# Performance work log

Measured on AMD Instinct MI355X. Metric: run time of the kernel, lower is better.

The kernel has to match this reference:

```python
import jax, jax.numpy as jnp
import numpy as np

DIM = 128
N = 8192
E = 262144
EPS = 1e-8  # torch.cosine_similarity eps


def setup_inputs() -> dict:
    key = jax.random.key(0)
    k1, k2, k3, k4 = jax.random.split(key, 4)
    x = jax.random.normal(k1, (N, DIM), dtype=jnp.float32)
    edge_index = jax.random.randint(k2, (2, E), 0, N, dtype=jnp.int32)
    # GCNConv parameters: linear weight (glorot-ish) and bias
    W_gcn = jax.random.normal(k3, (DIM, DIM), dtype=jnp.float32) / np.sqrt(DIM)
    b_gcn = jnp.zeros((DIM,), dtype=jnp.float32)
    return {"x": x, "edge_index": edge_index, "W_gcn": W_gcn, "b_gcn": b_gcn}


def _cosine_attention(x):
    # torch.cosine_similarity(x.unsqueeze(1), x.unsqueeze(0), dim=-1)
    # == (x @ x.T) / max(||x_i|| * ||x_j||, eps)
    nrm = jnp.sqrt(jnp.sum(x * x, axis=-1))                      # [N]
    denom = jnp.maximum(nrm[:, None] * nrm[None, :], EPS)        # [N, N]
    sim = (x @ x.T) / denom                                      # [N, N]
    return jax.nn.sigmoid(sim @ x)                               # [N, dim]


def _gcn_conv(x, edge_index, W, b):
    n = x.shape[0]
    xw = x @ W                                                   # [N, dim]
    # add self-loops
    loops = jnp.arange(n, dtype=edge_index.dtype)
    row = jnp.concatenate([edge_index[0], loops])                # source
    col = jnp.concatenate([edge_index[1], loops])                # target
    # symmetric normalization: deg computed on target nodes
    deg = jax.ops.segment_sum(jnp.ones_like(col, dtype=x.dtype), col, num_segments=n)
    dis = jnp.where(deg > 0, jax.lax.rsqrt(jnp.maximum(deg, 1.0)), 0.0)
    dis = jnp.where(deg > 0, deg ** -0.5, 0.0)
    norm = dis[row] * dis[col]                                   # [E+N]
    msgs = xw[row] * norm[:, None]                               # [E+N, dim]
    out = jax.ops.segment_sum(msgs, col, num_segments=n)         # [N, dim]
    return out + b


def reference(x, edge_index, W_gcn, b_gcn):
    att = _cosine_attention(x)
    g = _gcn_conv(x, edge_index, W_gcn, b_gcn)
    return g * att
```

## Files before the change

### kernel.cpp

```cpp
#include <hip/hip_runtime.h>
#include <math.h>

#define NN   8192
#define DIM  128
#define NE   262144
#define XB   128
#define HBH  64
#define HEB  (NE / HBH)
#define PBP  64
#define PEB  (NE / PBP)
#define RWB  32
#define BK   16
#define XSS  132
#define SMEMF 8448

static __device__ __forceinline__ unsigned short f2bf(float f) {
  unsigned int u = __float_as_uint(f);
  return (unsigned short)((u + 0x7FFFu + ((u >> 16) & 1u)) >> 16);
}
static __device__ __forceinline__ float bf2f(unsigned int h) {
  return __uint_as_float(h << 16);
}


static __device__ void ph_xtx(int u, int tid, float* smem,
    const float* __restrict__ x, float* __restrict__ rinv,
    float* __restrict__ Mpart) {
  float* xs  = smem;
  float* rvs = smem + 64 * DIM;
  int row0 = u * 64;
  const float4* xsrc = (const float4*)(x + (size_t)row0 * DIM);
  float4* xdst = (float4*)xs;
  #pragma unroll
  for (int i = 0; i < 8; ++i) xdst[tid + 256 * i] = xsrc[tid + 256 * i];
  __syncthreads();
  int rr = tid >> 2, q = tid & 3;
  const float4* xr = (const float4*)&xs[rr * DIM + q * 32];
  float ss = 0.f;
  #pragma unroll
  for (int i = 0; i < 8; ++i) {
    float4 v = xr[i];
    ss += v.x * v.x + v.y * v.y + v.z * v.z + v.w * v.w;
  }
  ss += __shfl_xor(ss, 1);
  ss += __shfl_xor(ss, 2);
  if (q == 0) { float rv = 1.0f / sqrtf(ss); rvs[rr] = rv; rinv[row0 + rr] = rv; }
  __syncthreads();

  int ty = tid >> 4, tx = tid & 15;
  float acc[8][8];
  #pragma unroll
  for (int i = 0; i < 8; ++i)
    #pragma unroll
    for (int j = 0; j < 8; ++j) acc[i][j] = 0.f;
  #pragma unroll 2
  for (int r = 0; r < 64; ++r) {
    float4 a0 = *(const float4*)&xs[r * DIM + ty * 4];
    float4 a1 = *(const float4*)&xs[r * DIM + 64 + ty * 4];
    float4 b0 = *(const float4*)&xs[r * DIM + tx * 4];
    float4 b1 = *(const float4*)&xs[r * DIM + 64 + tx * 4];
    float rv = rvs[r];
    float a[8] = {a0.x * rv, a0.y * rv, a0.z * rv, a0.w * rv,
                  a1.x * rv, a1.y * rv, a1.z * rv, a1.w * rv};
    float b[8] = {b0.x, b0.y, b0.z, b0.w, b1.x, b1.y, b1.z, b1.w};
    #pragma unroll
    for (int i = 0; i < 8; ++i)
      #pragma unroll
      for (int j = 0; j < 8; ++j) acc[i][j] += a[i] * b[j];
  }
  float* o = Mpart + (size_t)u * (DIM * DIM);
  #pragma unroll
  for (int i = 0; i < 8; ++i) {
    int row = (i < 4) ? (ty * 4 + i) : (64 + ty * 4 + (i - 4));
    *(float4*)&o[row * DIM + tx * 4]      = make_float4(acc[i][0], acc[i][1], acc[i][2], acc[i][3]);
    *(float4*)&o[row * DIM + 64 + tx * 4] = make_float4(acc[i][4], acc[i][5], acc[i][6], acc[i][7]);
  }
}

static __device__ void ph_hist(int h, int tid, int* ldeg,
    const int* __restrict__ ei, int* __restrict__ gcnt, int* __restrict__ slot) {
  int4* lz = (int4*)ldeg;
  #pragma unroll
  for (int i = tid; i < NN / 4; i += 256) lz[i] = make_int4(0, 0, 0, 0);
  __syncthreads();
  int e0 = h * HEB + tid * 16;
  int4 c0 = *(const int4*)(ei + NE + e0);
  int4 c1 = *(const int4*)(ei + NE + e0 + 4);
  int4 c2 = *(const int4*)(ei + NE + e0 + 8);
  int4 c3 = *(const int4*)(ei + NE + e0 + 12);
  int r0  = atomicAdd(&ldeg[c0.x], 1);
  int r1  = atomicAdd(&ldeg[c0.y], 1);
  int r2  = atomicAdd(&ldeg[c0.z], 1);
  int r3  = atomicAdd(&ldeg[c0.w], 1);
  int r4  = atomicAdd(&ldeg[c1.x], 1);
  int r5  = atomicAdd(&ldeg[c1.y], 1);
  int r6  = atomicAdd(&ldeg[c1.z], 1);
  int r7  = atomicAdd(&ldeg[c1.w], 1);
  int r8  = atomicAdd(&ldeg[c2.x], 1);
  int r9  = atomicAdd(&ldeg[c2.y], 1);
  int r10 = atomicAdd(&ldeg[c2.z], 1);
  int r11 = atomicAdd(&ldeg[c2.w], 1);
  int r12 = atomicAdd(&ldeg[c3.x], 1);
  int r13 = atomicAdd(&ldeg[c3.y], 1);
  int r14 = atomicAdd(&ldeg[c3.z], 1);
  int r15 = atomicAdd(&ldeg[c3.w], 1);
  __syncthreads();
  int binb = tid * 32;
  #pragma unroll
  for (int i = 0; i < 8; ++i) {
    int4 v = *(int4*)&ldeg[binb + i * 4];
    if (v.x) ldeg[binb + i * 4 + 0] = atomicAdd(&gcnt[binb + i * 4 + 0], v.x);
    if (v.y) ldeg[binb + i * 4 + 1] = atomicAdd(&gcnt[binb + i * 4 + 1], v.y);
    if (v.z) ldeg[binb + i * 4 + 2] = atomicAdd(&gcnt[binb + i * 4 + 2], v.z);
    if (v.w) ldeg[binb + i * 4 + 3] = atomicAdd(&gcnt[binb + i * 4 + 3], v.w);
  }
  __syncthreads();
  int4 s0 = make_int4(ldeg[c0.x] + r0,  ldeg[c0.y] + r1,  ldeg[c0.z] + r2,  ldeg[c0.w] + r3);
  int4 s1 = make_int4(ldeg[c1.x] + r4,  ldeg[c1.y] + r5,  ldeg[c1.z] + r6,  ldeg[c1.w] + r7);
  int4 s2 = make_int4(ldeg[c2.x] + r8,  ldeg[c2.y] + r9,  ldeg[c2.z] + r10, ldeg[c2.w] + r11);
  int4 s3 = make_int4(ldeg[c3.x] + r12, ldeg[c3.y] + r13, ldeg[c3.z] + r14, ldeg[c3.w] + r15);
  *(int4*)(slot + e0)      = s0;
  *(int4*)(slot + e0 + 4)  = s1;
  *(int4*)(slot + e0 + 8)  = s2;
  *(int4*)(slot + e0 + 12) = s3;
}

static __device__ void ph_mred(int u, int tid, float* smem,
    const float* __restrict__ Mpart, float* __restrict__ Mmat) {
  int j0 = u * 64;
  int jj = tid & 63, sub = tid >> 6;
  const float* mp = Mpart + (size_t)(sub * 32) * (DIM * DIM) + j0;
  float s = 0.f;
  #pragma unroll 4
  for (int k = 0; k < 32; ++k) s += mp[(size_t)k * (DIM * DIM) + jj];
  smem[sub * 64 + jj] = s;
  __syncthreads();
  if (tid < 64)
    Mmat[j0 + tid] = smem[tid] + smem[64 + tid] + smem[128 + tid] + smem[192 + tid];
}

static __device__ void ph_scan(int tid, int* wsum,
    const int* __restrict__ gcnt, int* __restrict__ offs, float* __restrict__ dis) {
  int lane = tid & 63, wave = tid >> 6;
  const int4* g4 = (const int4*)gcnt;
  int s = 0;
  #pragma unroll
  for (int i = 0; i < 8; ++i) { int4 v = g4[tid * 8 + i]; s += v.x + v.y + v.z + v.w; }
  int sc = s;
  #pragma unroll
  for (int off = 1; off < 64; off <<= 1) {
    int v = __shfl_up(sc, off);
    if (lane >= off) sc += v;
  }
  if (lane == 63) wsum[wave] = sc;
  __syncthreads();
  if (wave == 0 && lane < 4) {
    int v = wsum[lane];
    #pragma unroll
    for (int off = 1; off < 4; off <<= 1) {
      int u = __shfl_up(v, off);
      if (lane >= off) v += u;
    }
    wsum[lane] = v;
  }
  __syncthreads();
  int run = (wave ? wsum[wave - 1] : 0) + sc - s;
  #pragma unroll
  for (int i = 0; i < 8; ++i) {
    int4 v = g4[tid * 8 + i];
    int4 o;
    o.x = run; run += v.x;
    o.y = run; run += v.y;
    o.z = run; run += v.z;
    o.w = run; run += v.w;
    *(int4*)&offs[tid * 32 + i * 4] = o;
    float4 d;
    d.x = rsqrtf((float)(v.x + 1)); d.y = rsqrtf((float)(v.y + 1));
    d.z = rsqrtf((float)(v.z + 1)); d.w = rsqrtf((float)(v.w + 1));
    *(float4*)&dis[tid * 32 + i * 4] = d;
  }
}

static __device__ void ph_gemm(int u, int tid, float* smem,
    const float* __restrict__ x, const float* __restrict__ W,
    const float* __restrict__ Mmat, const float* __restrict__ rinv,
    const float* __restrict__ dis, unsigned short* __restrict__ xws,
    float* __restrict__ att) {
  float* xs  = smem;
  float* Wl  = smem + 4224;
  float* Ml  = smem + 6272;
  float* rvs = smem + 8320;
  float* dss = smem + 8352;
  int row0 = u * RWB;
  #pragma unroll
  for (int i = 0; i < 4; ++i) {
    int fidx = i * 256 + tid;
    int row = fidx >> 5, c4 = fidx & 31;
    ((float4*)(xs + row * XSS))[c4] =
        ((const float4*)(x + (size_t)(row0 + row) * DIM))[c4];
  }
  if (tid < RWB) { rvs[tid] = rinv[row0 + tid]; dss[tid] = dis[row0 + tid]; }

  int ry = tid >> 5, tx = tid & 31;
  int r0 = ry * 4;
  float4 aw[4], am[4];
  #pragma unroll
  for (int j = 0; j < 4; ++j) { aw[j] = make_float4(0,0,0,0); am[j] = make_float4(0,0,0,0); }

  for (int kk = 0; kk < DIM; kk += BK) {
    __syncthreads();
    const float4* Ws = (const float4*)(W + (size_t)kk * DIM);
    const float4* Ms = (const float4*)(Mmat + (size_t)kk * DIM);
    ((float4*)Wl)[tid]       = Ws[tid];
    ((float4*)Wl)[tid + 256] = Ws[tid + 256];
    ((float4*)Ml)[tid]       = Ms[tid];
    ((float4*)Ml)[tid + 256] = Ms[tid + 256];
    __syncthreads();
    #pragma unroll
    for (int k4 = 0; k4 < BK; k4 += 4) {
      float4 xf[4];
      #pragma unroll
      for (int j = 0; j < 4; ++j)
        xf[j] = *(const float4*)&xs[(r0 + j) * XSS + kk + k4];
      #pragma unroll
      for (int k = 0; k < 4; ++k) {
        float4 wv = *(const float4*)&Wl[(k4 + k) * DIM + tx * 4];
        float4 mv = *(const float4*)&Ml[(k4 + k) * DIM + tx * 4];
        #pragma unroll
        for (int j = 0; j < 4; ++j) {
          float xv = ((const float*)&xf[j])[k];
          aw[j].x += xv * wv.x; aw[j].y += xv * wv.y;
          aw[j].z += xv * wv.z; aw[j].w += xv * wv.w;
          am[j].x += xv * mv.x; am[j].y += xv * mv.y;
          am[j].z += xv * mv.z; am[j].w += xv * mv.w;
        }
      }
    }
  }
  #pragma unroll
  for (int j = 0; j < 4; ++j) {
    int row = row0 + r0 + j;
    float rv = rvs[r0 + j], ds = dss[r0 + j];
    size_t o = (size_t)row * DIM + tx * 4;
    ushort4 wb;
    wb.x = f2bf(aw[j].x * ds); wb.y = f2bf(aw[j].y * ds);
    wb.z = f2bf(aw[j].z * ds); wb.w = f2bf(aw[j].w * ds);
    *(ushort4*)&xws[o] = wb;
    float4 g;
    g.x = 1.0f / (1.0f + __expf(-am[j].x * rv));
    g.y = 1.0f / (1.0f + __expf(-am[j].y * rv));
    g.z = 1.0f / (1.0f + __expf(-am[j].z * rv));
    g.w = 1.0f / (1.0f + __expf(-am[j].w * rv));
    *(float4*)&att[o] = g;
  }
}

static __device__ void ph_place(int u, int tid,
    const int* __restrict__ ei, const int* __restrict__ offs,
    const int* __restrict__ slot, int* __restrict__ sorted) {
  int e0 = u * PEB + tid * 16;
  #pragma unroll
  for (int i = 0; i < 4; ++i) {
    int4 sv = *(const int4*)(ei + e0 + i * 4);
    int4 cv = *(const int4*)(ei + NE + e0 + i * 4);
    int4 sl = *(const int4*)(slot + e0 + i * 4);
    sorted[offs[cv.x] + sl.x] = sv.x;
    sorted[offs[cv.y] + sl.y] = sv.y;
    sorted[offs[cv.z] + sl.z] = sv.z;
    sorted[offs[cv.w] + sl.w] = sv.w;
  }
}

__global__ __launch_bounds__(256) void k_pA(const float* __restrict__ x,
    const int* __restrict__ ei, float* __restrict__ rinv,
    float* __restrict__ Mpart, int* __restrict__ gcnt, int* __restrict__ slot) {
  __shared__ float smem[SMEMF];
  int u = blockIdx.x, tid = threadIdx.x;
  if (u < XB) ph_xtx(u, tid, smem, x, rinv, Mpart);
  else        ph_hist(u - XB, tid, (int*)smem, ei, gcnt, slot);
}
__global__ __launch_bounds__(256) void k_pB(const float* __restrict__ Mpart,
    float* __restrict__ Mmat, const int* __restrict__ gcnt,
    int* __restrict__ offs, float* __restrict__ dis) {
  __shared__ float smem[SMEMF];
  int u = blockIdx.x, tid = threadIdx.x;
  if (u < 256) ph_mred(u, tid, smem, Mpart, Mmat);
  else         ph_scan(tid, (int*)smem, gcnt, offs, dis);
}
__global__ __launch_bounds__(256) void k_pC(const float* __restrict__ x,
    const float* __restrict__ W, const float* __restrict__ Mmat,
    const float* __restrict__ rinv, const float* __restrict__ dis,
    const int* __restrict__ ei, const int* __restrict__ offs,
    const int* __restrict__ slot, int* __restrict__ sorted,
    unsigned short* __restrict__ xws, float* __restrict__ att) {
  __shared__ float smem[SMEMF];
  int u = blockIdx.x, tid = threadIdx.x;
  if (u < NN / RWB) ph_gemm(u, tid, smem, x, W, Mmat, rinv, dis, xws, att);
  else              ph_place(u - NN / RWB, tid, ei, offs, slot, sorted);
}
__global__ __launch_bounds__(64) void k_pD(const int* __restrict__ offs,
    const int* __restrict__ gcnt, const float* __restrict__ dis,
    const unsigned short* __restrict__ xws, const float* __restrict__ att,
    const float* __restrict__ bias, const int* __restrict__ sorted,
    float* __restrict__ out) {
  int c = blockIdx.x, t = threadIdx.x;
  int base = offs[c];
  int cnt  = gcnt[c];
  const unsigned int* xw2 = (const unsigned int*)xws;
  unsigned int sv = xw2[(size_t)c * 64 + t];
  float acc0 = bf2f(sv & 0xffffu), acc1 = bf2f(sv >> 16);
  int k = 0;
  for (; k + 8 <= cnt; k += 8) {
    int4 i0 = *(const int4*)(sorted + base + k);
    int4 i1 = *(const int4*)(sorted + base + k + 4);
    unsigned int v0 = xw2[(size_t)i0.x * 64 + t];
    unsigned int v1 = xw2[(size_t)i0.y * 64 + t];
    unsigned int v2 = xw2[(size_t)i0.z * 64 + t];
    unsigned int v3 = xw2[(size_t)i0.w * 64 + t];
    unsigned int v4 = xw2[(size_t)i1.x * 64 + t];
    unsigned int v5 = xw2[(size_t)i1.y * 64 + t];
    unsigned int v6 = xw2[(size_t)i1.z * 64 + t];
    unsigned int v7 = xw2[(size_t)i1.w * 64 + t];
    acc0 += bf2f(v0 & 0xffffu) + bf2f(v1 & 0xffffu) + bf2f(v2 & 0xffffu) + bf2f(v3 & 0xffffu)
          + bf2f(v4 & 0xffffu) + bf2f(v5 & 0xffffu) + bf2f(v6 & 0xffffu) + bf2f(v7 & 0xffffu);
    acc1 += bf2f(v0 >> 16) + bf2f(v1 >> 16) + bf2f(v2 >> 16) + bf2f(v3 >> 16)
          + bf2f(v4 >> 16) + bf2f(v5 >> 16) + bf2f(v6 >> 16) + bf2f(v7 >> 16);
  }
  for (; k + 4 <= cnt; k += 4) {
    int4 i0 = *(const int4*)(sorted + base + k);
    unsigned int v0 = xw2[(size_t)i0.x * 64 + t];
    unsigned int v1 = xw2[(size_t)i0.y * 64 + t];
    unsigned int v2 = xw2[(size_t)i0.z * 64 + t];
    unsigned int v3 = xw2[(size_t)i0.w * 64 + t];
    acc0 += bf2f(v0 & 0xffffu) + bf2f(v1 & 0xffffu) + bf2f(v2 & 0xffffu) + bf2f(v3 & 0xffffu);
    acc1 += bf2f(v0 >> 16) + bf2f(v1 >> 16) + bf2f(v2 >> 16) + bf2f(v3 >> 16);
  }
  for (; k < cnt; ++k) {
    unsigned int v = xw2[(size_t)sorted[base + k] * 64 + t];
    acc0 += bf2f(v & 0xffffu);
    acc1 += bf2f(v >> 16);
  }
  float dc = dis[c];
  float2 at = ((const float2*)att)[(size_t)c * 64 + t];
  float2 bs = ((const float2*)bias)[t];
  float2 o;
  o.x = (acc0 * dc + bs.x) * at.x;
  o.y = (acc1 * dc + bs.y) * at.y;
  ((float2*)out)[(size_t)c * 64 + t] = o;
}

extern "C" void kernel_launch(void* const* d_in, const int* in_sizes, int n_in,
                              void* d_out, int out_size, void* d_ws, size_t ws_size,
                              hipStream_t stream) {
  const float* x  = (const float*)d_in[0];
  const int*   ei = (const int*)  d_in[1];
  const float* W  = (const float*)d_in[2];
  const float* b  = (const float*)d_in[3];
  float* out = (float*)d_out;

  unsigned short* xws = (unsigned short*)d_ws;
  float* att   = (float*)(xws + (size_t)NN * DIM);
  float* Mpart = att + (size_t)NN * DIM;
  float* Mmat  = Mpart + (size_t)XB * DIM * DIM;
  float* rinv  = Mmat + DIM * DIM;
  float* dis   = rinv + NN;
  int*   gcnt  = (int*)(dis + NN);
  int*   offs  = gcnt + NN;
  int*   slot  = offs + NN;
  int*   sorted= slot + NE;

  hipMemsetAsync(gcnt, 0, NN * sizeof(int), stream);

  k_pA<<<XB + HBH, 256, 0, stream>>>(x, ei, rinv, Mpart, gcnt, slot);
  k_pB<<<257, 256, 0, stream>>>(Mpart, Mmat, gcnt, offs, dis);
  k_pC<<<NN / RWB + PBP, 256, 0, stream>>>(x, W, Mmat, rinv, dis, ei, offs,
                                           slot, sorted, xws, att);
  k_pD<<<NN, 64, 0, stream>>>(offs, gcnt, dis, xws, att, b, sorted, out);
}
```

Measured before the change: 112.1 us.

## Move Gram and projection GEMMs to bf16 MFMA with pre-transposed concatenated weights

Replaces the scalar FP32 x^T·diag(rinv)·x Gram computation and the x·[W|M] projection with bf16 MFMA 16x16x32 instructions using swizzled LDS layouts. W and the reduced M are packed and transposed into a single bf16 B-matrix in the reduction kernel, so the projection GEMM loads its B operands straight into registers. The Gram phase now uses 64 blocks of 128 rows instead of 128 blocks of 64, which halves the partial-sum reduction. This lowers the cost of the two dense GEMM stages but rounds x, W and M to bf16, which adds error to the attention and GCN outputs.

New measurement: 106.1 us. 1.06x faster.

```diff
diff --git a/kernel.cpp b/kernel.cpp
--- a/kernel.cpp
+++ b/kernel.cpp
@@ -4,15 +4,17 @@
 #define NN   8192
 #define DIM  128
 #define NE   262144
-#define XB   128
+#define XU   64
+#define JCH  128
 #define HBH  64
 #define HEB  (NE / HBH)
 #define PBP  64
 #define PEB  (NE / PBP)
-#define RWB  32
-#define BK   16
-#define XSS  132
-#define SMEMF 8448
+#define GU   128
+#define GR   64
+
+typedef __attribute__((ext_vector_type(8))) short bf16x8;
+typedef __attribute__((ext_vector_type(4))) float f32x4;
 
 static __device__ __forceinline__ unsigned short f2bf(float f) {
   unsigned int u = __float_as_uint(f);
@@ -21,60 +23,72 @@
 static __device__ __forceinline__ float bf2f(unsigned int h) {
   return __uint_as_float(h << 16);
 }
-
-
-static __device__ void ph_xtx(int u, int tid, float* smem,
+static __device__ __forceinline__ unsigned int pk2(float a, float b) {
+  return (unsigned int)f2bf(a) | ((unsigned int)f2bf(b) << 16);
+}
+
+
+static __device__ void ph_xtx(int u, int tid, char* smem,
     const float* __restrict__ x, float* __restrict__ rinv,
     float* __restrict__ Mpart) {
-  float* xs  = smem;
-  float* rvs = smem + 64 * DIM;
-  int row0 = u * 64;
-  const float4* xsrc = (const float4*)(x + (size_t)row0 * DIM);
-  float4* xdst = (float4*)xs;
-  #pragma unroll
-  for (int i = 0; i < 8; ++i) xdst[tid + 256 * i] = xsrc[tid + 256 * i];
-  __syncthreads();
-  int rr = tid >> 2, q = tid & 3;
-  const float4* xr = (const float4*)&xs[rr * DIM + q * 32];
+  char* XTs = smem;
+  char* XTu = smem + 32768;
+  int j0 = u * JCH;
+  int jl = tid >> 1, half = tid & 1;
+  const float4* xr = (const float4*)(x + (size_t)(j0 + jl) * DIM + half * 64);
   float ss = 0.f;
   #pragma unroll
-  for (int i = 0; i < 8; ++i) {
+  for (int i = 0; i < 16; ++i) {
     float4 v = xr[i];
     ss += v.x * v.x + v.y * v.y + v.z * v.z + v.w * v.w;
   }
   ss += __shfl_xor(ss, 1);
-  ss += __shfl_xor(ss, 2);
-  if (q == 0) { float rv = 1.0f / sqrtf(ss); rvs[rr] = rv; rinv[row0 + rr] = rv; }
-  __syncthreads();
-
-  int ty = tid >> 4, tx = tid & 15;
-  float acc[8][8];
-  #pragma unroll
-  for (int i = 0; i < 8; ++i)
-    #pragma unroll
-    for (int j = 0; j < 8; ++j) acc[i][j] = 0.f;
-  #pragma unroll 2
-  for (int r = 0; r < 64; ++r) {
-    float4 a0 = *(const float4*)&xs[r * DIM + ty * 4];
-    float4 a1 = *(const float4*)&xs[r * DIM + 64 + ty * 4];
-    float4 b0 = *(const float4*)&xs[r * DIM + tx * 4];
-    float4 b1 = *(const float4*)&xs[r * DIM + 64 + tx * 4];
-    float rv = rvs[r];
-    float a[8] = {a0.x * rv, a0.y * rv, a0.z * rv, a0.w * rv,
-                  a1.x * rv, a1.y * rv, a1.z * rv, a1.w * rv};
-    float b[8] = {b0.x, b0.y, b0.z, b0.w, b1.x, b1.y, b1.z, b1.w};
-    #pragma unroll
-    for (int i = 0; i < 8; ++i)
+  float rv = 1.0f / sqrtf(ss);
+  if (half == 0) rinv[j0 + jl] = rv;
+  #pragma unroll
+  for (int c4 = 0; c4 < 16; ++c4) {
+    float4 v = xr[c4];
+    #pragma unroll
+    for (int i = 0; i < 4; ++i) {
+      int d = half * 64 + c4 * 4 + i;
+      float f = ((const float*)&v)[i];
+      int off = d * 256 + ((jl * 2) ^ ((d & 7) << 4));
+      *(unsigned short*)(XTs + off) = f2bf(f * rv);
+      *(unsigned short*)(XTu + off) = f2bf(f);
+    }
+  }
+  __syncthreads();
+
+  int w = tid >> 6, lane = tid & 63;
+  int l15 = lane & 15, g16 = (lane >> 4) * 16, swz = (lane & 7) << 4;
+  f32x4 acc[2][8];
+  #pragma unroll
+  for (int dt = 0; dt < 2; ++dt)
+    #pragma unroll
+    for (int ct = 0; ct < 8; ++ct) acc[dt][ct] = (f32x4){0.f, 0.f, 0.f, 0.f};
+  #pragma unroll
+  for (int ks = 0; ks < 4; ++ks) {
+    int ko = (ks * 64 + g16) ^ swz;
+    bf16x8 a0 = *(const bf16x8*)(XTs + (w * 32 + l15) * 256 + ko);
+    bf16x8 a1 = *(const bf16x8*)(XTs + (w * 32 + 16 + l15) * 256 + ko);
+    #pragma unroll
+    for (int ct = 0; ct < 8; ++ct) {
+      bf16x8 b = *(const bf16x8*)(XTu + (ct * 16 + l15) * 256 + ko);
+      acc[0][ct] = __builtin_amdgcn_mfma_f32_16x16x32_bf16(a0, b, acc[0][ct], 0, 0, 0);
+      acc[1][ct] = __builtin_amdgcn_mfma_f32_16x16x32_bf16(a1, b, acc[1][ct], 0, 0, 0);
+    }
+  }
+  float* o = Mpart + (size_t)u * (DIM * DIM);
+  #pragma unroll
+  for (int dt = 0; dt < 2; ++dt)
+    #pragma unroll
+    for (int ct = 0; ct < 8; ++ct)
       #pragma unroll
-      for (int j = 0; j < 8; ++j) acc[i][j] += a[i] * b[j];
-  }
-  float* o = Mpart + (size_t)u * (DIM * DIM);
-  #pragma unroll
-  for (int i = 0; i < 8; ++i) {
-    int row = (i < 4) ? (ty * 4 + i) : (64 + ty * 4 + (i - 4));
-    *(float4*)&o[row * DIM + tx * 4]      = make_float4(acc[i][0], acc[i][1], acc[i][2], acc[i][3]);
-    *(float4*)&o[row * DIM + 64 + tx * 4] = make_float4(acc[i][4], acc[i][5], acc[i][6], acc[i][7]);
-  }
+      for (int r = 0; r < 4; ++r) {
+        int row = w * 32 + dt * 16 + (lane >> 4) * 4 + r;
+        int col = ct * 16 + l15;
+        o[row * DIM + col] = acc[dt][ct][r];
+      }
 }
 
 static __device__ void ph_hist(int h, int tid, int* ldeg,
@@ -125,18 +139,43 @@
   *(int4*)(slot + e0 + 12) = s3;
 }
 
-static __device__ void ph_mred(int u, int tid, float* smem,
-    const float* __restrict__ Mpart, float* __restrict__ Mmat) {
+static __device__ void ph_mred(int u, int tid, float* smemf,
+    const float* __restrict__ Mpart, unsigned short* __restrict__ Bg) {
   int j0 = u * 64;
   int jj = tid & 63, sub = tid >> 6;
-  const float* mp = Mpart + (size_t)(sub * 32) * (DIM * DIM) + j0;
+  const float* mp = Mpart + (size_t)(sub * 16) * (DIM * DIM) + j0;
   float s = 0.f;
   #pragma unroll 4
-  for (int k = 0; k < 32; ++k) s += mp[(size_t)k * (DIM * DIM) + jj];
-  smem[sub * 64 + jj] = s;
-  __syncthreads();
-  if (tid < 64)
-    Mmat[j0 + tid] = smem[tid] + smem[64 + tid] + smem[128 + tid] + smem[192 + tid];
+  for (int k = 0; k < 16; ++k) s += mp[(size_t)k * (DIM * DIM) + jj];
+  smemf[sub * 64 + jj] = s;
+  __syncthreads();
+  if (tid < 64) {
+    float v = smemf[tid] + smemf[64 + tid] + smemf[128 + tid] + smemf[192 + tid];
+    int flat = j0 + tid;
+    int row = flat >> 7, col = flat & 127;
+    Bg[(size_t)(128 + row) * DIM + col] = f2bf(v);
+  }
+}
+
+static __device__ void ph_wt(int b, int tid, float* smemf,
+    const float* __restrict__ W, unsigned short* __restrict__ Bg) {
+  float4* dst = (float4*)smemf;
+  const float4* src = (const float4*)(W + (size_t)b * 32 * DIM);
+  #pragma unroll
+  for (int i = 0; i < 4; ++i) dst[tid + 256 * i] = src[tid + 256 * i];
+  __syncthreads();
+  int j = tid >> 1, kh = (tid & 1) * 16;
+  uint4 p0, p1;
+  p0.x = pk2(smemf[(kh + 0) * DIM + j],  smemf[(kh + 1) * DIM + j]);
+  p0.y = pk2(smemf[(kh + 2) * DIM + j],  smemf[(kh + 3) * DIM + j]);
+  p0.z = pk2(smemf[(kh + 4) * DIM + j],  smemf[(kh + 5) * DIM + j]);
+  p0.w = pk2(smemf[(kh + 6) * DIM + j],  smemf[(kh + 7) * DIM + j]);
+  p1.x = pk2(smemf[(kh + 8) * DIM + j],  smemf[(kh + 9) * DIM + j]);
+  p1.y = pk2(smemf[(kh + 10) * DIM + j], smemf[(kh + 11) * DIM + j]);
+  p1.z = pk2(smemf[(kh + 12) * DIM + j], smemf[(kh + 13) * DIM + j]);
+  p1.w = pk2(smemf[(kh + 14) * DIM + j], smemf[(kh + 15) * DIM + j]);
+  uint4* op = (uint4*)(Bg + (size_t)j * DIM + b * 32 + kh);
+  op[0] = p0; op[1] = p1;
 }
 
 static __device__ void ph_scan(int tid, int* wsum,
@@ -181,78 +220,74 @@
   }
 }
 
-static __device__ void ph_gemm(int u, int tid, float* smem,
-    const float* __restrict__ x, const float* __restrict__ W,
-    const float* __restrict__ Mmat, const float* __restrict__ rinv,
-    const float* __restrict__ dis, unsigned short* __restrict__ xws,
-    float* __restrict__ att) {
-  float* xs  = smem;
-  float* Wl  = smem + 4224;
-  float* Ml  = smem + 6272;
-  float* rvs = smem + 8320;
-  float* dss = smem + 8352;
-  int row0 = u * RWB;
+static __device__ void ph_gemm(int u, int tid, char* smem,
+    const float* __restrict__ x, const unsigned short* __restrict__ Bg,
+    const float* __restrict__ rinv, const float* __restrict__ dis,
+    unsigned short* __restrict__ xws, float* __restrict__ att) {
+  char* A = smem;
+  float* rvs = (float*)(smem + 16384);
+  float* dss = rvs + 64;
+  int row0 = u * GR;
   #pragma unroll
   for (int i = 0; i < 4; ++i) {
-    int fidx = i * 256 + tid;
-    int row = fidx >> 5, c4 = fidx & 31;
-    ((float4*)(xs + row * XSS))[c4] =
-        ((const float4*)(x + (size_t)(row0 + row) * DIM))[c4];
-  }
-  if (tid < RWB) { rvs[tid] = rinv[row0 + tid]; dss[tid] = dis[row0 + tid]; }
-
-  int ry = tid >> 5, tx = tid & 31;
-  int r0 = ry * 4;
-  float4 aw[4], am[4];
-  #pragma unroll
-  for (int j = 0; j < 4; ++j) { aw[j] = make_float4(0,0,0,0); am[j] = make_float4(0,0,0,0); }
-
-  for (int kk = 0; kk < DIM; kk += BK) {
-    __syncthreads();
-    const float4* Ws = (const float4*)(W + (size_t)kk * DIM);
-    const float4* Ms = (const float4*)(Mmat + (size_t)kk * DIM);
-    ((float4*)Wl)[tid]       = Ws[tid];
-    ((float4*)Wl)[tid + 256] = Ws[tid + 256];
-    ((float4*)Ml)[tid]       = Ms[tid];
-    ((float4*)Ml)[tid + 256] = Ms[tid + 256];
-    __syncthreads();
-    #pragma unroll
-    for (int k4 = 0; k4 < BK; k4 += 4) {
-      float4 xf[4];
+    int c = tid + 256 * i;
+    int row = c >> 4, kc = c & 15;
+    const float4* s = (const float4*)(x + (size_t)(row0 + row) * DIM + kc * 8);
+    float4 v0 = s[0], v1 = s[1];
+    uint4 p;
+    p.x = pk2(v0.x, v0.y); p.y = pk2(v0.z, v0.w);
+    p.z = pk2(v1.x, v1.y); p.w = pk2(v1.z, v1.w);
+    *(uint4*)(A + row * 256 + ((kc * 16) ^ ((row & 7) << 4))) = p;
+  }
+  if (tid < 64) { rvs[tid] = rinv[row0 + tid]; dss[tid] = dis[row0 + tid]; }
+
+  int w = tid >> 6, lane = tid & 63;
+  int l15 = lane & 15, g16 = (lane >> 4) * 16, swz = (lane & 7) << 4;
+  bf16x8 breg[4][4];
+  const char* Bgb = (const char*)Bg;
+  #pragma unroll
+  for (int ct = 0; ct < 4; ++ct) {
+    int j = w * 64 + ct * 16 + l15;
+    #pragma unroll
+    for (int ks = 0; ks < 4; ++ks)
+      breg[ct][ks] = *(const bf16x8*)(Bgb + j * 256 + ks * 64 + g16);
+  }
+  __syncthreads();
+
+  f32x4 acc[4][4];
+  #pragma unroll
+  for (int rt = 0; rt < 4; ++rt)
+    #pragma unroll
+    for (int ct = 0; ct < 4; ++ct) acc[rt][ct] = (f32x4){0.f, 0.f, 0.f, 0.f};
+  #pragma unroll
+  for (int rt = 0; rt < 4; ++rt) {
+    #pragma unroll
+    for (int ks = 0; ks < 4; ++ks) {
+      bf16x8 a = *(const bf16x8*)(A + (rt * 16 + l15) * 256 + ((ks * 64 + g16) ^ swz));
       #pragma unroll
-      for (int j = 0; j < 4; ++j)
-        xf[j] = *(const float4*)&xs[(r0 + j) * XSS + kk + k4];
+      for (int ct = 0; ct < 4; ++ct)
+        acc[rt][ct] = __builtin_amdgcn_mfma_f32_16x16x32_bf16(a, breg[ct][ks], acc[rt][ct], 0, 0, 0);
+    }
+  }
+
+  bool isW = (w < 2);
+  #pragma unroll
+  for (int rt = 0; rt < 4; ++rt)
+    #pragma unroll
+    for (int ct = 0; ct < 4; ++ct)
       #pragma unroll
-      for (int k = 0; k < 4; ++k) {
-        float4 wv = *(const float4*)&Wl[(k4 + k) * DIM + tx * 4];
-        float4 mv = *(const float4*)&Ml[(k4 + k) * DIM + tx * 4];
-        #pragma unroll
-        for (int j = 0; j < 4; ++j) {
-          float xv = ((const float*)&xf[j])[k];
-          aw[j].x += xv * wv.x; aw[j].y += xv * wv.y;
-          aw[j].z += xv * wv.z; aw[j].w += xv * wv.w;
-          am[j].x += xv * mv.x; am[j].y += xv * mv.y;
-          am[j].z += xv * mv.z; am[j].w += xv * mv.w;
+      for (int r = 0; r < 4; ++r) {
+        int rl = rt * 16 + (lane >> 4) * 4 + r;
+        int row = row0 + rl;
+        int col = w * 64 + ct * 16 + l15;
+        float v = acc[rt][ct][r];
+        if (isW) {
+          xws[(size_t)row * DIM + col] = f2bf(v * dss[rl]);
+        } else {
+          float gv = 1.0f / (1.0f + __expf(-v * rvs[rl]));
+          att[(size_t)row * DIM + (col - 128)] = gv;
         }
       }
-    }
-  }
-  #pragma unroll
-  for (int j = 0; j < 4; ++j) {
-    int row = row0 + r0 + j;
-    float rv = rvs[r0 + j], ds = dss[r0 + j];
-    size_t o = (size_t)row * DIM + tx * 4;
-    ushort4 wb;
-    wb.x = f2bf(aw[j].x * ds); wb.y = f2bf(aw[j].y * ds);
-    wb.z = f2bf(aw[j].z * ds); wb.w = f2bf(aw[j].w * ds);
-    *(ushort4*)&xws[o] = wb;
-    float4 g;
-    g.x = 1.0f / (1.0f + __expf(-am[j].x * rv));
-    g.y = 1.0f / (1.0f + __expf(-am[j].y * rv));
-    g.z = 1.0f / (1.0f + __expf(-am[j].z * rv));
-    g.w = 1.0f / (1.0f + __expf(-am[j].w * rv));
-    *(float4*)&att[o] = g;
-  }
 }
 
 static __device__ void ph_place(int u, int tid,
@@ -274,29 +309,30 @@
 __global__ __launch_bounds__(256) void k_pA(const float* __restrict__ x,
     const int* __restrict__ ei, float* __restrict__ rinv,
     float* __restrict__ Mpart, int* __restrict__ gcnt, int* __restrict__ slot) {
-  __shared__ float smem[SMEMF];
+  __shared__ float smem[16512];
   int u = blockIdx.x, tid = threadIdx.x;
-  if (u < XB) ph_xtx(u, tid, smem, x, rinv, Mpart);
-  else        ph_hist(u - XB, tid, (int*)smem, ei, gcnt, slot);
+  if (u < XU) ph_xtx(u, tid, (char*)smem, x, rinv, Mpart);
+  else        ph_hist(u - XU, tid, (int*)smem, ei, gcnt, slot);
 }
 __global__ __launch_bounds__(256) void k_pB(const float* __restrict__ Mpart,
-    float* __restrict__ Mmat, const int* __restrict__ gcnt,
-    int* __restrict__ offs, float* __restrict__ dis) {
-  __shared__ float smem[SMEMF];
+    const float* __restrict__ W, unsigned short* __restrict__ Bg,
+    const int* __restrict__ gcnt, int* __restrict__ offs, float* __restrict__ dis) {
+  __shared__ float smem[4224];
   int u = blockIdx.x, tid = threadIdx.x;
-  if (u < 256) ph_mred(u, tid, smem, Mpart, Mmat);
-  else         ph_scan(tid, (int*)smem, gcnt, offs, dis);
+  if (u < 256)      ph_mred(u, tid, smem, Mpart, Bg);
+  else if (u == 256) ph_scan(tid, (int*)smem, gcnt, offs, dis);
+  else              ph_wt(u - 257, tid, smem, W, Bg);
 }
 __global__ __launch_bounds__(256) void k_pC(const float* __restrict__ x,
-    const float* __restrict__ W, const float* __restrict__ Mmat,
-    const float* __restrict__ rinv, const float* __restrict__ dis,
-    const int* __restrict__ ei, const int* __restrict__ offs,
-    const int* __restrict__ slot, int* __restrict__ sorted,
-    unsigned short* __restrict__ xws, float* __restrict__ att) {
-  __shared__ float smem[SMEMF];
+    const unsigned short* __restrict__ Bg, const float* __restrict__ rinv,
+    const float* __restrict__ dis, const int* __restrict__ ei,
+    const int* __restrict__ offs, const int* __restrict__ slot,
+    int* __restrict__ sorted, unsigned short* __restrict__ xws,
+    float* __restrict__ att) {
+  __shared__ float smem[4224];
   int u = blockIdx.x, tid = threadIdx.x;
-  if (u < NN / RWB) ph_gemm(u, tid, smem, x, W, Mmat, rinv, dis, xws, att);
-  else              ph_place(u - NN / RWB, tid, ei, offs, slot, sorted);
+  if (u < GU) ph_gemm(u, tid, (char*)smem, x, Bg, rinv, dis, xws, att);
+  else        ph_place(u - GU, tid, ei, offs, slot, sorted);
 }
 __global__ __launch_bounds__(64) void k_pD(const int* __restrict__ offs,
     const int* __restrict__ gcnt, const float* __restrict__ dis,
@@ -360,9 +396,9 @@
 
   unsigned short* xws = (unsigned short*)d_ws;
   float* att   = (float*)(xws + (size_t)NN * DIM);
-  float* Mpart = att + (size_t)NN * DIM;
-  float* Mmat  = Mpart + (size_t)XB * DIM * DIM;
-  float* rinv  = Mmat + DIM * DIM;
+  unsigned short* Bg = (unsigned short*)(att + (size_t)NN * DIM);
+  float* Mpart = (float*)(Bg + 256 * DIM);
+  float* rinv  = Mpart + (size_t)XU * DIM * DIM;
   float* dis   = rinv + NN;
   int*   gcnt  = (int*)(dis + NN);
   int*   offs  = gcnt + NN;
@@ -371,9 +407,9 @@
 
   hipMemsetAsync(gcnt, 0, NN * sizeof(int), stream);
 
-  k_pA<<<XB + HBH, 256, 0, stream>>>(x, ei, rinv, Mpart, gcnt, slot);
-  k_pB<<<257, 256, 0, stream>>>(Mpart, Mmat, gcnt, offs, dis);
-  k_pC<<<NN / RWB + PBP, 256, 0, stream>>>(x, W, Mmat, rinv, dis, ei, offs,
-                                           slot, sorted, xws, att);
+  k_pA<<<XU + HBH, 256, 0, stream>>>(x, ei, rinv, Mpart, gcnt, slot);
+  k_pB<<<261, 256, 0, stream>>>(Mpart, W, Bg, gcnt, offs, dis);
+  k_pC<<<GU + PBP, 256, 0, stream>>>(x, Bg, rinv, dis, ei, offs, slot, sorted,
+                                     xws, att);
   k_pD<<<NN, 64, 0, stream>>>(offs, gcnt, dis, xws, att, b, sorted, out);
 }
```
